# Kernel optimization log

Hardware: AMD Instinct MI355X
Metric: run time of the kernel (lower is better)

Reference implementation:

```python
import jax, jax.numpy as jnp
import numpy as np

B, N, TOKEN_DIM, HIDDEN = 4, 2048, 512, 128
LN_EPS = 1e-5
NEG_SLOPE = 0.01  # torch LeakyReLU default


def setup_inputs() -> dict:
    key = jax.random.key(0)
    ks = jax.random.split(key, 6)
    s_fc = 1.0 / np.sqrt(TOKEN_DIM)
    s_at = 1.0 / np.sqrt(2 * HIDDEN)
    return {
        "token_embedding": jax.random.normal(ks[0], (B, N, TOKEN_DIM), jnp.float32),
        "fc_w": jax.random.uniform(ks[1], (HIDDEN, TOKEN_DIM), jnp.float32, -s_fc, s_fc),
        "fc_b": jax.random.uniform(ks[2], (HIDDEN,), jnp.float32, -s_fc, s_fc),
        "attn_w": jax.random.uniform(ks[3], (1, 2 * HIDDEN), jnp.float32, -s_at, s_at),
        "attn_b": jax.random.uniform(ks[4], (1,), jnp.float32, -s_at, s_at),
        "ln_g": jnp.ones((HIDDEN,), jnp.float32),
        "ln_b": jnp.zeros((HIDDEN,), jnp.float32),
    }


def reference(token_embedding, fc_w, fc_b, attn_w, attn_b, ln_g, ln_b):
    # h = LayerNorm(Linear(x))  -> [B, N, H]
    h = jnp.einsum("bnt,ht->bnh", token_embedding, fc_w) + fc_b
    mu = jnp.mean(h, axis=-1, keepdims=True)
    var = jnp.mean(jnp.square(h - mu), axis=-1, keepdims=True)
    h = ln_g * (h - mu) * jax.lax.rsqrt(var + LN_EPS) + ln_b

    # Original: concat_h[b,i,j] = [h[b,j], h[b,i]] then attn_fc (dropout is identity at eval).
    # Algebraically: score[b,i,j] = h[b,j].w_row + h[b,i].w_col + bias
    w_row = attn_w[0, :HIDDEN]
    w_col = attn_w[0, HIDDEN:]
    s_row = h @ w_row  # [B, N]
    s_col = h @ w_col  # [B, N]
    e = s_col[:, :, None] + s_row[:, None, :] + attn_b[0]  # [B, N, N]
    e = jnp.where(e >= 0, e, NEG_SLOPE * e)  # LeakyReLU
    a = jax.nn.softmax(e, axis=-1)
    h_prime = jnp.einsum("bij,bjh->bih", a, h)
    return h_prime
```

## Files before the change

### kernel.cpp

```cpp
#include <hip/hip_runtime.h>

#define NB      4
#define NTOK    2048
#define TOKDIM  512
#define HID     128
#define NROWS   (NB * NTOK)
#define LN_EPS  1e-5f
#define NEG_SLOPE 0.01f

typedef short bf16x8 __attribute__((ext_vector_type(8)));
typedef float f32x4  __attribute__((ext_vector_type(4)));

static __device__ __forceinline__ unsigned short f2bf(float f) {
    union { float f; unsigned int i; } v; v.f = f;
    unsigned int i = v.i;
    i += 0x7FFFu + ((i >> 16) & 1u);
    return (unsigned short)(i >> 16);
}

__global__ __launch_bounds__(256) void k_prep(const float* __restrict__ W,
                                              unsigned short* __restrict__ Wb) {
    const int g = blockIdx.x * 256 + threadIdx.x;
    float4 v = *(const float4*)(W + (size_t)g * 4);
    ushort4 o;
    o.x = f2bf(v.x); o.y = f2bf(v.y); o.z = f2bf(v.z); o.w = f2bf(v.w);
    *(ushort4*)(Wb + (size_t)g * 4) = o;
}

__global__ __launch_bounds__(512) void k_fused(const float* __restrict__ X,
                                               const unsigned short* __restrict__ Wb,
                                               const float* __restrict__ fcb,
                                               const float* __restrict__ attnw,
                                               const float* __restrict__ attnb,
                                               const float* __restrict__ lng,
                                               const float* __restrict__ lnb,
                                               unsigned short* __restrict__ hT,
                                               float* __restrict__ srow,
                                               float* __restrict__ cc) {
    __shared__ char smem[16640 + 16 * 132 * 4];
    unsigned short* ldsX = (unsigned short*)smem;
    unsigned short* ldsT = (unsigned short*)smem;
    float* hfull = (float*)(smem + 16640);

    const int tid  = threadIdx.x;
    const int wv   = tid >> 6;
    const int lane = tid & 63;
    const int m    = lane & 15;
    const int q    = lane >> 4;
    const int rowbase = blockIdx.x * 16;
    const int nbase   = wv * 16;

    {
        const int r  = tid >> 5;
        const int c0 = (tid & 31) * 16;
        const float* xp = X + (size_t)(rowbase + r) * TOKDIM + c0;
        bf16x8 v0, v1;
#pragma unroll
        for (int u = 0; u < 8; ++u) v0[u] = (short)f2bf(xp[u]);
#pragma unroll
        for (int u = 0; u < 8; ++u) v1[u] = (short)f2bf(xp[8 + u]);
        *(bf16x8*)&ldsX[r * 520 + c0]     = v0;
        *(bf16x8*)&ldsX[r * 520 + c0 + 8] = v1;
    }
    __syncthreads();

    const unsigned short* wp = Wb + (size_t)(nbase + m) * TOKDIM + q * 8;
    f32x4 acc = {0.f, 0.f, 0.f, 0.f};
#pragma unroll
    for (int kk = 0; kk < TOKDIM / 32; ++kk) {
        bf16x8 a = *(const bf16x8*)&ldsX[m * 520 + kk * 32 + q * 8];
        bf16x8 b = *(const bf16x8*)(wp + kk * 32);
        acc = __builtin_amdgcn_mfma_f32_16x16x32_bf16(a, b, acc, 0, 0, 0);
    }

    {
        const float bias = fcb[nbase + m];
#pragma unroll
        for (int r = 0; r < 4; ++r)
            hfull[(q * 4 + r) * 132 + nbase + m] = acc[r] + bias;
    }
    __syncthreads();

    {
        const int r   = tid >> 5;
        const int l32 = tid & 31;
        const int c0  = l32 * 4;
        float4 hv = *(const float4*)&hfull[r * 132 + c0];
        float v[4] = {hv.x, hv.y, hv.z, hv.w};

        float s  = v[0] + v[1] + v[2] + v[3];
        float ss = v[0]*v[0] + v[1]*v[1] + v[2]*v[2] + v[3]*v[3];
#pragma unroll
        for (int d = 1; d < 32; d <<= 1) {
            s  += __shfl_xor(s,  d, 64);
            ss += __shfl_xor(ss, d, 64);
        }
        float mu  = s * (1.f / HID);
        float var = ss * (1.f / HID) - mu * mu;
        float rs  = rsqrtf(var + LN_EPS);

        float n[4], sr = 0.f, sc = 0.f;
#pragma unroll
        for (int k = 0; k < 4; ++k) {
            n[k] = lng[c0 + k] * (v[k] - mu) * rs + lnb[c0 + k];
            sr += n[k] * attnw[c0 + k];
            sc += n[k] * attnw[HID + c0 + k];
            ldsT[(c0 + k) * 20 + r] = f2bf(n[k]);
        }
#pragma unroll
        for (int d = 1; d < 32; d <<= 1) {
            sr += __shfl_xor(sr, d, 64);
            sc += __shfl_xor(sc, d, 64);
        }
        if (l32 == 0) {
            int grow = rowbase + r;
            srow[grow] = sr;
            cc[grow]   = sc + attnb[0];
        }
    }
    __syncthreads();

    {
        const int d  = tid >> 2;
        const int j4 = (tid & 3) * 4;
        const int b    = blockIdx.x >> 7;
        const int jblk = (blockIdx.x & 127) * 16;
        ushort4 o;
        o.x = ldsT[d * 20 + j4 + 0];
        o.y = ldsT[d * 20 + j4 + 1];
        o.z = ldsT[d * 20 + j4 + 2];
        o.w = ldsT[d * 20 + j4 + 3];
        *(ushort4*)(hT + ((size_t)(b * HID + d)) * NTOK + jblk + j4) = o;
    }
}

__global__ __launch_bounds__(512) void k_attn(const unsigned short* __restrict__ hT,
                                              const float* __restrict__ srow,
                                              const float* __restrict__ cc,
                                              float* __restrict__ out) {
    __shared__ unsigned short pP[2][32][264];
    __shared__ float pDen[32][16];
    __shared__ float denv[32];

    const int tid  = threadIdx.x;
    const int wv   = tid >> 6;
    const int lane = tid & 63;
    const int m    = lane & 15;
    const int q    = lane >> 4;
    const int rowbase = blockIdx.x * 32;
    const int b    = blockIdx.x >> 6;
    const int dbase = wv * 16;

    const int i_loc = tid >> 4;
    const int jseg  = (tid & 15) * 16;
    const float ci  = cc[rowbase + i_loc];
    const float* sp = srow + (size_t)b * NTOK + jseg;

    const unsigned short* hp =
        hT + ((size_t)(b * HID + dbase + m)) * NTOK + q * 8;

    f32x4 acc0 = {0.f, 0.f, 0.f, 0.f};
    f32x4 acc1 = {0.f, 0.f, 0.f, 0.f};
    float lsum = 0.f;

    float4 s0 = *(const float4*)(sp);
    float4 s1 = *(const float4*)(sp + 4);
    float4 s2 = *(const float4*)(sp + 8);
    float4 s3 = *(const float4*)(sp + 12);
    bf16x8 bcur[8], bnxt[8];
#pragma unroll
    for (int s = 0; s < 8; ++s) bcur[s] = *(const bf16x8*)(hp + s * 32);

#pragma unroll
    for (int ch = 0; ch < 8; ++ch) {
        {
            float sv[16] = {s0.x, s0.y, s0.z, s0.w, s1.x, s1.y, s1.z, s1.w,
                            s2.x, s2.y, s2.z, s2.w, s3.x, s3.y, s3.z, s3.w};
            bf16x8 v0, v1;
#pragma unroll
            for (int u = 0; u < 8; ++u) {
                float z = ci + sv[u];
                z = fmaxf(z, NEG_SLOPE * z);
                float p = __expf(z);
                lsum += p;
                v0[u] = (short)f2bf(p);
            }
#pragma unroll
            for (int u = 0; u < 8; ++u) {
                float z = ci + sv[8 + u];
                z = fmaxf(z, NEG_SLOPE * z);
                float p = __expf(z);
                lsum += p;
                v1[u] = (short)f2bf(p);
            }
            *(bf16x8*)&pP[ch & 1][i_loc][jseg]     = v0;
            *(bf16x8*)&pP[ch & 1][i_loc][jseg + 8] = v1;
        }

        if (ch < 7) {
            const float* spn = sp + (ch + 1) * 256;
            s0 = *(const float4*)(spn);
            s1 = *(const float4*)(spn + 4);
            s2 = *(const float4*)(spn + 8);
            s3 = *(const float4*)(spn + 12);
            const unsigned short* hpn = hp + (ch + 1) * 256;
#pragma unroll
            for (int s = 0; s < 8; ++s) bnxt[s] = *(const bf16x8*)(hpn + s * 32);
        }

        __syncthreads();

#pragma unroll
        for (int s = 0; s < 8; ++s) {
            bf16x8 a0 = *(const bf16x8*)&pP[ch & 1][m][s * 32 + q * 8];
            bf16x8 a1 = *(const bf16x8*)&pP[ch & 1][16 + m][s * 32 + q * 8];
            acc0 = __builtin_amdgcn_mfma_f32_16x16x32_bf16(a0, bcur[s], acc0, 0, 0, 0);
            acc1 = __builtin_amdgcn_mfma_f32_16x16x32_bf16(a1, bcur[s], acc1, 0, 0, 0);
        }

#pragma unroll
        for (int s = 0; s < 8; ++s) bcur[s] = bnxt[s];
    }

    pDen[i_loc][tid & 15] = lsum;
    __syncthreads();
    if (tid < 32) {
        float d = 0.f;
#pragma unroll
        for (int k = 0; k < 16; ++k) d += pDen[tid][k];
        denv[tid] = 1.f / d;
    }
    __syncthreads();

#pragma unroll
    for (int r = 0; r < 4; ++r) {
        int r0 = q * 4 + r;
        out[(size_t)(rowbase + r0) * HID + dbase + m]      = acc0[r] * denv[r0];
        out[(size_t)(rowbase + 16 + r0) * HID + dbase + m] = acc1[r] * denv[16 + r0];
    }
}

extern "C" void kernel_launch(void* const* d_in, const int* in_sizes, int n_in,
                              void* d_out, int out_size, void* d_ws, size_t ws_size,
                              hipStream_t stream) {
    const float* X     = (const float*)d_in[0];
    const float* W     = (const float*)d_in[1];
    const float* fcb   = (const float*)d_in[2];
    const float* attnw = (const float*)d_in[3];
    const float* attnb = (const float*)d_in[4];
    const float* lng   = (const float*)d_in[5];
    const float* lnb   = (const float*)d_in[6];
    float* out = (float*)d_out;

    char* ws = (char*)d_ws;
    unsigned short* hT   = (unsigned short*)ws;
    float*          srow = (float*)(ws + 2u * 1024 * 1024);
    float*          cchd = (float*)(ws + 2u * 1024 * 1024 + 32u * 1024);
    unsigned short* Wb   = (unsigned short*)(ws + 2u * 1024 * 1024 + 64u * 1024);

    k_prep <<<64, 256, 0, stream>>>(W, Wb);
    k_fused<<<NROWS / 16, 512, 0, stream>>>(X, Wb, fcb, attnw, attnb, lng, lnb,
                                            hT, srow, cchd);
    k_attn <<<NROWS / 32, 512, 0, stream>>>(hT, srow, cchd, out);
}
```

Before: 105.8 us.

## Software-pipeline softmax chunk production in attn and double k_fused row tile

In k_attn, the next chunk's exponentials are now written into the alternate LDS buffer before the current chunk's MFMAs run. This leaves one barrier per chunk, placed after the MFMAs, so exp work overlaps the matrix multiply. Separately, k_fused now handles 32 rows per block with 1024 threads, halving the grid and reusing each W fragment load across twice as many rows. The larger blocks use more LDS and may lower occupancy.

```diff
diff --git a/kernel.cpp b/kernel.cpp
--- a/kernel.cpp
+++ b/kernel.cpp
@@ -27,28 +27,29 @@
     *(ushort4*)(Wb + (size_t)g * 4) = o;
 }
 
-__global__ __launch_bounds__(512) void k_fused(const float* __restrict__ X,
-                                               const unsigned short* __restrict__ Wb,
-                                               const float* __restrict__ fcb,
-                                               const float* __restrict__ attnw,
-                                               const float* __restrict__ attnb,
-                                               const float* __restrict__ lng,
-                                               const float* __restrict__ lnb,
-                                               unsigned short* __restrict__ hT,
-                                               float* __restrict__ srow,
-                                               float* __restrict__ cc) {
-    __shared__ char smem[16640 + 16 * 132 * 4];
+__global__ __launch_bounds__(1024) void k_fused(const float* __restrict__ X,
+                                                const unsigned short* __restrict__ Wb,
+                                                const float* __restrict__ fcb,
+                                                const float* __restrict__ attnw,
+                                                const float* __restrict__ attnb,
+                                                const float* __restrict__ lng,
+                                                const float* __restrict__ lnb,
+                                                unsigned short* __restrict__ hT,
+                                                float* __restrict__ srow,
+                                                float* __restrict__ cc) {
+    __shared__ char smem[33280 + 32 * 132 * 4];
     unsigned short* ldsX = (unsigned short*)smem;
     unsigned short* ldsT = (unsigned short*)smem;
-    float* hfull = (float*)(smem + 16640);
-
-    const int tid  = threadIdx.x;
-    const int wv   = tid >> 6;
-    const int lane = tid & 63;
-    const int m    = lane & 15;
-    const int q    = lane >> 4;
-    const int rowbase = blockIdx.x * 16;
-    const int nbase   = wv * 16;
+    float* hfull = (float*)(smem + 33280);
+
+    const int tid   = threadIdx.x;
+    const int wv    = tid >> 6;
+    const int lane  = tid & 63;
+    const int m     = lane & 15;
+    const int q     = lane >> 4;
+    const int rowbase = blockIdx.x * 32;
+    const int nbase   = (wv & 7) * 16;
+    const int rhalf   = (wv >> 3) * 16;
 
     {
         const int r  = tid >> 5;
@@ -68,7 +69,7 @@
     f32x4 acc = {0.f, 0.f, 0.f, 0.f};
 #pragma unroll
     for (int kk = 0; kk < TOKDIM / 32; ++kk) {
-        bf16x8 a = *(const bf16x8*)&ldsX[m * 520 + kk * 32 + q * 8];
+        bf16x8 a = *(const bf16x8*)&ldsX[(rhalf + m) * 520 + kk * 32 + q * 8];
         bf16x8 b = *(const bf16x8*)(wp + kk * 32);
         acc = __builtin_amdgcn_mfma_f32_16x16x32_bf16(a, b, acc, 0, 0, 0);
     }
@@ -77,7 +78,7 @@
         const float bias = fcb[nbase + m];
 #pragma unroll
         for (int r = 0; r < 4; ++r)
-            hfull[(q * 4 + r) * 132 + nbase + m] = acc[r] + bias;
+            hfull[(rhalf + q * 4 + r) * 132 + nbase + m] = acc[r] + bias;
     }
     __syncthreads();
 
@@ -105,7 +106,7 @@
             n[k] = lng[c0 + k] * (v[k] - mu) * rs + lnb[c0 + k];
             sr += n[k] * attnw[c0 + k];
             sc += n[k] * attnw[HID + c0 + k];
-            ldsT[(c0 + k) * 20 + r] = f2bf(n[k]);
+            ldsT[(c0 + k) * 36 + r] = f2bf(n[k]);
         }
 #pragma unroll
         for (int d = 1; d < 32; d <<= 1) {
@@ -121,17 +122,44 @@
     __syncthreads();
 
     {
-        const int d  = tid >> 2;
-        const int j4 = (tid & 3) * 4;
-        const int b    = blockIdx.x >> 7;
-        const int jblk = (blockIdx.x & 127) * 16;
+        const int d  = tid >> 3;
+        const int j4 = (tid & 7) * 4;
+        const int b    = blockIdx.x >> 6;
+        const int jblk = (blockIdx.x & 63) * 32;
         ushort4 o;
-        o.x = ldsT[d * 20 + j4 + 0];
-        o.y = ldsT[d * 20 + j4 + 1];
-        o.z = ldsT[d * 20 + j4 + 2];
-        o.w = ldsT[d * 20 + j4 + 3];
+        o.x = ldsT[d * 36 + j4 + 0];
+        o.y = ldsT[d * 36 + j4 + 1];
+        o.z = ldsT[d * 36 + j4 + 2];
+        o.w = ldsT[d * 36 + j4 + 3];
         *(ushort4*)(hT + ((size_t)(b * HID + d)) * NTOK + jblk + j4) = o;
     }
+}
+
+static __device__ __forceinline__ void produce_chunk(
+        unsigned short* __restrict__ dst,
+        float ci, float4 s0, float4 s1, float4 s2, float4 s3,
+        float& lsum) {
+    float sv[16] = {s0.x, s0.y, s0.z, s0.w, s1.x, s1.y, s1.z, s1.w,
+                    s2.x, s2.y, s2.z, s2.w, s3.x, s3.y, s3.z, s3.w};
+    bf16x8 v0, v1;
+#pragma unroll
+    for (int u = 0; u < 8; ++u) {
+        float z = ci + sv[u];
+        z = fmaxf(z, NEG_SLOPE * z);
+        float p = __expf(z);
+        lsum += p;
+        v0[u] = (short)f2bf(p);
+    }
+#pragma unroll
+    for (int u = 0; u < 8; ++u) {
+        float z = ci + sv[8 + u];
+        z = fmaxf(z, NEG_SLOPE * z);
+        float p = __expf(z);
+        lsum += p;
+        v1[u] = (short)f2bf(p);
+    }
+    *(bf16x8*)dst       = v0;
+    *(bf16x8*)(dst + 8) = v1;
 }
 
 __global__ __launch_bounds__(512) void k_attn(const unsigned short* __restrict__ hT,
@@ -171,44 +199,35 @@
 #pragma unroll
     for (int s = 0; s < 8; ++s) bcur[s] = *(const bf16x8*)(hp + s * 32);
 
+    produce_chunk(&pP[0][i_loc][jseg], ci, s0, s1, s2, s3, lsum);
+
+    float4 n0, n1, n2, n3;
+    {
+        const float* spn = sp + 256;
+        n0 = *(const float4*)(spn);
+        n1 = *(const float4*)(spn + 4);
+        n2 = *(const float4*)(spn + 8);
+        n3 = *(const float4*)(spn + 12);
+    }
+
+    __syncthreads();
+
 #pragma unroll
     for (int ch = 0; ch < 8; ++ch) {
-        {
-            float sv[16] = {s0.x, s0.y, s0.z, s0.w, s1.x, s1.y, s1.z, s1.w,
-                            s2.x, s2.y, s2.z, s2.w, s3.x, s3.y, s3.z, s3.w};
-            bf16x8 v0, v1;
-#pragma unroll
-            for (int u = 0; u < 8; ++u) {
-                float z = ci + sv[u];
-                z = fmaxf(z, NEG_SLOPE * z);
-                float p = __expf(z);
-                lsum += p;
-                v0[u] = (short)f2bf(p);
+        if (ch < 7) {
+            produce_chunk(&pP[(ch + 1) & 1][i_loc][jseg], ci, n0, n1, n2, n3, lsum);
+
+            if (ch < 6) {
+                const float* spn = sp + (ch + 2) * 256;
+                n0 = *(const float4*)(spn);
+                n1 = *(const float4*)(spn + 4);
+                n2 = *(const float4*)(spn + 8);
+                n3 = *(const float4*)(spn + 12);
             }
-#pragma unroll
-            for (int u = 0; u < 8; ++u) {
-                float z = ci + sv[8 + u];
-                z = fmaxf(z, NEG_SLOPE * z);
-                float p = __expf(z);
-                lsum += p;
-                v1[u] = (short)f2bf(p);
-            }
-            *(bf16x8*)&pP[ch & 1][i_loc][jseg]     = v0;
-            *(bf16x8*)&pP[ch & 1][i_loc][jseg + 8] = v1;
-        }
-
-        if (ch < 7) {
-            const float* spn = sp + (ch + 1) * 256;
-            s0 = *(const float4*)(spn);
-            s1 = *(const float4*)(spn + 4);
-            s2 = *(const float4*)(spn + 8);
-            s3 = *(const float4*)(spn + 12);
             const unsigned short* hpn = hp + (ch + 1) * 256;
 #pragma unroll
             for (int s = 0; s < 8; ++s) bnxt[s] = *(const bf16x8*)(hpn + s * 32);
         }
-
-        __syncthreads();
 
 #pragma unroll
         for (int s = 0; s < 8; ++s) {
@@ -217,6 +236,8 @@
             acc0 = __builtin_amdgcn_mfma_f32_16x16x32_bf16(a0, bcur[s], acc0, 0, 0, 0);
             acc1 = __builtin_amdgcn_mfma_f32_16x16x32_bf16(a1, bcur[s], acc1, 0, 0, 0);
         }
+
+        __syncthreads();
 
 #pragma unroll
         for (int s = 0; s < 8; ++s) bcur[s] = bnxt[s];
@@ -259,7 +280,7 @@
     unsigned short* Wb   = (unsigned short*)(ws + 2u * 1024 * 1024 + 64u * 1024);
 
     k_prep <<<64, 256, 0, stream>>>(W, Wb);
-    k_fused<<<NROWS / 16, 512, 0, stream>>>(X, Wb, fcb, attnw, attnb, lng, lnb,
-                                            hT, srow, cchd);
+    k_fused<<<NROWS / 32, 1024, 0, stream>>>(X, Wb, fcb, attnw, attnb, lng, lnb,
+                                             hT, srow, cchd);
     k_attn <<<NROWS / 32, 512, 0, stream>>>(hT, srow, cchd, out);
 }
```

Result: no change. 105.6 us (median of 2 runs) (-0.2%).

## Software-pipeline softmax-weight generation for the next chunk with the current chunk's MFMAs

Applied to the files above, without the earlier changes.

Restructures the attention loop so the exp/LeakyReLU/bf16 conversion for chunk ch+1 is interleaved with the MFMA steps of chunk ch, writing into the other LDS buffer. A prologue produces chunk 0 before the loop, and the srow values are prefetched two chunks ahead. This hides transcendental ALU work behind matrix instructions and cuts the serial produce-then-consume phase per chunk. In exchange, register pressure rises from carrying the prefetched scores, the next-chunk B fragments and the partial bf16 vectors at the same time.

```diff
diff --git a/kernel.cpp b/kernel.cpp
--- a/kernel.cpp
+++ b/kernel.cpp
@@ -134,6 +134,33 @@
     }
 }
 
+static __device__ __forceinline__ void produce_chunk(
+        unsigned short* __restrict__ dst,
+        float ci, float4 s0, float4 s1, float4 s2, float4 s3,
+        float& lsum) {
+    float sv[16] = {s0.x, s0.y, s0.z, s0.w, s1.x, s1.y, s1.z, s1.w,
+                    s2.x, s2.y, s2.z, s2.w, s3.x, s3.y, s3.z, s3.w};
+    bf16x8 v0, v1;
+#pragma unroll
+    for (int u = 0; u < 8; ++u) {
+        float z = ci + sv[u];
+        z = fmaxf(z, NEG_SLOPE * z);
+        float p = __expf(z);
+        lsum += p;
+        v0[u] = (short)f2bf(p);
+    }
+#pragma unroll
+    for (int u = 0; u < 8; ++u) {
+        float z = ci + sv[8 + u];
+        z = fmaxf(z, NEG_SLOPE * z);
+        float p = __expf(z);
+        lsum += p;
+        v1[u] = (short)f2bf(p);
+    }
+    *(bf16x8*)dst       = v0;
+    *(bf16x8*)(dst + 8) = v1;
+}
+
 __global__ __launch_bounds__(512) void k_attn(const unsigned short* __restrict__ hT,
                                               const float* __restrict__ srow,
                                               const float* __restrict__ cc,
@@ -167,60 +194,78 @@
     float4 s1 = *(const float4*)(sp + 4);
     float4 s2 = *(const float4*)(sp + 8);
     float4 s3 = *(const float4*)(sp + 12);
-    bf16x8 bcur[8], bnxt[8];
+    bf16x8 bcur[8];
 #pragma unroll
     for (int s = 0; s < 8; ++s) bcur[s] = *(const bf16x8*)(hp + s * 32);
 
+    produce_chunk(&pP[0][i_loc][jseg], ci, s0, s1, s2, s3, lsum);
+
+    float4 n0, n1, n2, n3;
+    {
+        const float* spn = sp + 256;
+        n0 = *(const float4*)(spn);
+        n1 = *(const float4*)(spn + 4);
+        n2 = *(const float4*)(spn + 8);
+        n3 = *(const float4*)(spn + 12);
+    }
+
+    __syncthreads();
+
+#define ASTEP(s, f0, f1, V, e)                                                  \
+    {                                                                           \
+        bf16x8 a0 = *(const bf16x8*)&pP[ch & 1][m][(s) * 32 + q * 8];           \
+        bf16x8 a1 = *(const bf16x8*)&pP[ch & 1][16 + m][(s) * 32 + q * 8];      \
+        acc0 = __builtin_amdgcn_mfma_f32_16x16x32_bf16(a0, bcur[s], acc0, 0, 0, 0); \
+        acc1 = __builtin_amdgcn_mfma_f32_16x16x32_bf16(a1, bcur[s], acc1, 0, 0, 0); \
+        if (ch < 7) {                                                           \
+            float z0 = ci + (f0); z0 = fmaxf(z0, NEG_SLOPE * z0);               \
+            float p0 = __expf(z0); lsum += p0;                                  \
+            float z1 = ci + (f1); z1 = fmaxf(z1, NEG_SLOPE * z1);               \
+            float p1 = __expf(z1); lsum += p1;                                  \
+            V[e]     = (short)f2bf(p0);                                         \
+            V[e + 1] = (short)f2bf(p1);                                         \
+        }                                                                       \
+    }
+
 #pragma unroll
     for (int ch = 0; ch < 8; ++ch) {
-        {
-            float sv[16] = {s0.x, s0.y, s0.z, s0.w, s1.x, s1.y, s1.z, s1.w,
-                            s2.x, s2.y, s2.z, s2.w, s3.x, s3.y, s3.z, s3.w};
-            bf16x8 v0, v1;
-#pragma unroll
-            for (int u = 0; u < 8; ++u) {
-                float z = ci + sv[u];
-                z = fmaxf(z, NEG_SLOPE * z);
-                float p = __expf(z);
-                lsum += p;
-                v0[u] = (short)f2bf(p);
+        bf16x8 bnxt[8];
+        if (ch < 7) {
+            const unsigned short* hpn = hp + (ch + 1) * 256;
+#pragma unroll
+            for (int s = 0; s < 8; ++s) bnxt[s] = *(const bf16x8*)(hpn + s * 32);
+        }
+
+        bf16x8 v0, v1;
+        ASTEP(0, n0.x, n0.y, v0, 0)
+        ASTEP(1, n0.z, n0.w, v0, 2)
+        ASTEP(2, n1.x, n1.y, v0, 4)
+        ASTEP(3, n1.z, n1.w, v0, 6)
+        ASTEP(4, n2.x, n2.y, v1, 0)
+        ASTEP(5, n2.z, n2.w, v1, 2)
+        ASTEP(6, n3.x, n3.y, v1, 4)
+        ASTEP(7, n3.z, n3.w, v1, 6)
+
+        if (ch < 7) {
+            *(bf16x8*)&pP[(ch + 1) & 1][i_loc][jseg]     = v0;
+            *(bf16x8*)&pP[(ch + 1) & 1][i_loc][jseg + 8] = v1;
+            if (ch < 6) {
+                const float* spn = sp + (ch + 2) * 256;
+                n0 = *(const float4*)(spn);
+                n1 = *(const float4*)(spn + 4);
+                n2 = *(const float4*)(spn + 8);
+                n3 = *(const float4*)(spn + 12);
             }
-#pragma unroll
-            for (int u = 0; u < 8; ++u) {
-                float z = ci + sv[8 + u];
-                z = fmaxf(z, NEG_SLOPE * z);
-                float p = __expf(z);
-                lsum += p;
-                v1[u] = (short)f2bf(p);
-            }
-            *(bf16x8*)&pP[ch & 1][i_loc][jseg]     = v0;
-            *(bf16x8*)&pP[ch & 1][i_loc][jseg + 8] = v1;
-        }
+        }
+
+        __syncthreads();
 
         if (ch < 7) {
-            const float* spn = sp + (ch + 1) * 256;
-            s0 = *(const float4*)(spn);
-            s1 = *(const float4*)(spn + 4);
-            s2 = *(const float4*)(spn + 8);
-            s3 = *(const float4*)(spn + 12);
-            const unsigned short* hpn = hp + (ch + 1) * 256;
-#pragma unroll
-            for (int s = 0; s < 8; ++s) bnxt[s] = *(const bf16x8*)(hpn + s * 32);
-        }
-
-        __syncthreads();
-
-#pragma unroll
-        for (int s = 0; s < 8; ++s) {
-            bf16x8 a0 = *(const bf16x8*)&pP[ch & 1][m][s * 32 + q * 8];
-            bf16x8 a1 = *(const bf16x8*)&pP[ch & 1][16 + m][s * 32 + q * 8];
-            acc0 = __builtin_amdgcn_mfma_f32_16x16x32_bf16(a0, bcur[s], acc0, 0, 0, 0);
-            acc1 = __builtin_amdgcn_mfma_f32_16x16x32_bf16(a1, bcur[s], acc1, 0, 0, 0);
-        }
-
-#pragma unroll
-        for (int s = 0; s < 8; ++s) bcur[s] = bnxt[s];
-    }
+#pragma unroll
+            for (int s = 0; s < 8; ++s) bcur[s] = bnxt[s];
+        }
+    }
+#undef ASTEP
 
     pDen[i_loc][tid & 15] = lsum;
     __syncthreads();
```

Result: no change. 106.2 us (+0.4%).
